# Kernel tuning notes

Hardware: AMD Instinct MI355X
Metric: run time of the kernel (lower is better)

Reference implementation:

```python
import jax, jax.numpy as jnp
import numpy as np

N = 12288      # nodes
E = 393216     # edges (avg degree 32)
D_IN = 512
D_H = 256      # interm_dim
D_Z = 64       # latent_dim


def setup_inputs() -> dict:
    key = jax.random.key(0)
    ks = jax.random.split(key, 9)
    X = jax.random.normal(ks[0], (N, D_IN), jnp.float32)
    edge_index = jax.random.randint(ks[1], (2, E), 0, N, dtype=jnp.int64)
    # GCNConv weights (glorot-ish scaling)
    W1 = jax.random.normal(ks[2], (D_IN, D_H), jnp.float32) / np.sqrt(D_IN)
    b1 = jnp.zeros((D_H,), jnp.float32)
    Wmu = jax.random.normal(ks[3], (D_H, D_Z), jnp.float32) / np.sqrt(D_H)
    bmu = jnp.zeros((D_Z,), jnp.float32)
    Wsig = jax.random.normal(ks[4], (D_H, 1), jnp.float32) / np.sqrt(D_H)
    bsig = jnp.zeros((1,), jnp.float32)
    # reparameterization noise (torch: Normal(0,1).sample(mus.size()))
    eps = jax.random.normal(ks[5], (N, D_Z), jnp.float32)
    return {"X": X, "edge_index": edge_index, "W1": W1, "b1": b1,
            "Wmu": Wmu, "bmu": bmu, "Wsig": Wsig, "bsig": bsig, "eps": eps}


def _gcn_conv(h_in, W, b, src, dst, norm):
    # GCNConv: linear transform then symmetric-normalized aggregation with self-loops
    h = h_in @ W + b                                   # [N, F_out]
    msg = h[src] * norm[src, None]                     # gather + scale
    agg = jax.ops.segment_sum(msg, dst, num_segments=N)
    # self-loop contribution: norm_i * norm_i * h_i
    return norm[:, None] * (agg + norm[:, None] * h)


def reference(X, edge_index, W1, b1, Wmu, bmu, Wsig, bsig, eps):
    src, dst = edge_index[0], edge_index[1]
    # degree of A + I (edge weight 1, plus self loop)
    deg = jax.ops.segment_sum(jnp.ones((E,), X.dtype), dst, num_segments=N) + 1.0
    norm = jax.lax.rsqrt(deg)                          # D^{-1/2}

    # encoder
    H = jax.nn.relu(_gcn_conv(X, W1, b1, src, dst, norm))   # [N, D_H]; dropout p=0.0
    mus = _gcn_conv(H, Wmu, bmu, src, dst, norm)            # [N, D_Z]
    logsigma2s = _gcn_conv(H, Wsig, bsig, src, dst, norm)   # [N, 1]

    # reparameterize
    sigmas = jnp.exp(0.5 * logsigma2s)                      # [N, 1]
    Z = mus + sigmas * eps                                  # [N, D_Z]

    # dense decoder
    ZZt = Z @ Z.T                                           # [N, N]
    return ZZt, mus, logsigma2s
```

## Files before the change

### kernel.cpp

```cpp
#include <hip/hip_runtime.h>

#define N_NODES 12288
#define N_EDGES 393216
#define DIN 512
#define DH 256
#define DZ 64

typedef __bf16 bf16x8 __attribute__((ext_vector_type(8)));
typedef float f32x4 __attribute__((ext_vector_type(4)));

static __device__ __forceinline__ unsigned short f2bf(float f) {
    unsigned int u = __float_as_uint(f);
    unsigned int r = (u + 0x7fffu + ((u >> 16) & 1u)) >> 16;
    return (unsigned short)r;
}
static __device__ __forceinline__ float bf2f(unsigned short u) {
    return __uint_as_float((unsigned int)u << 16);
}

__global__ __launch_bounds__(256) void k_prep(const float* __restrict__ X, unsigned short* __restrict__ Xb,
                                              const float* __restrict__ W1, unsigned short* __restrict__ W1T,
                                              const float* __restrict__ Wmu, unsigned short* __restrict__ WmuT,
                                              const int* __restrict__ dst, int* __restrict__ deg) {
    int b = blockIdx.x;
    if (b < 6144) {
        int i = b * 256 + threadIdx.x;
        float4 v = ((const float4*)X)[i];
        ushort4 o;
        o.x = f2bf(v.x); o.y = f2bf(v.y); o.z = f2bf(v.z); o.w = f2bf(v.w);
        ((ushort4*)Xb)[i] = o;
    } else if (b < 6656) {
        int i = (b - 6144) * 256 + threadIdx.x;
        int c = i >> 9, k = i & 511;
        W1T[i] = f2bf(W1[k * DH + c]);
    } else if (b < 6720) {
        int i = (b - 6656) * 256 + threadIdx.x;
        int c = i >> 8, k = i & 255;
        WmuT[i] = f2bf(Wmu[k * DZ + c]);
    } else {
        int e = (b - 6720) * 256 + threadIdx.x;
        atomicAdd(&deg[dst[e]], 1);
    }
}

__global__ __launch_bounds__(1024) void k_scan(const int* __restrict__ cnt, int* __restrict__ rp,
                                               float* __restrict__ norm) {
    __shared__ int sp[1024];
    int t = threadIdx.x;
    int base = t * 12;
    int loc[12];
    int s = 0;
#pragma unroll
    for (int j = 0; j < 12; ++j) {
        int c = cnt[base + j];
        norm[base + j] = rsqrtf((float)c + 1.0f);
        loc[j] = s; s += c;
    }
    sp[t] = s;
    __syncthreads();
    for (int off = 1; off < 1024; off <<= 1) {
        int v = (t >= off) ? sp[t - off] : 0;
        __syncthreads();
        sp[t] += v;
        __syncthreads();
    }
    int pre = (t == 0) ? 0 : sp[t - 1];
#pragma unroll
    for (int j = 0; j < 12; ++j) rp[base + j] = pre + loc[j];
    if (t == 1023) rp[N_NODES] = sp[1023];
}

__global__ __launch_bounds__(256) void k_scatter(const int* __restrict__ src, const int* __restrict__ dst,
                                                 const int* __restrict__ rp, int* __restrict__ cursor,
                                                 int* __restrict__ ssrc) {
    int e = blockIdx.x * 256 + threadIdx.x;
    int d = dst[e];
    int pos = atomicAdd(&cursor[d], 1);
    ssrc[rp[d] + pos] = src[e];
}

__global__ __launch_bounds__(256) void k_gemm1(const unsigned short* __restrict__ Xb,
                                               const unsigned short* __restrict__ W1T,
                                               const float* __restrict__ b1, const float* __restrict__ norm,
                                               unsigned short* __restrict__ g1) {
    int wid = threadIdx.x >> 6;
    int lane = threadIdx.x & 63;
    int ln = lane & 15, kg = lane >> 4;
    int rb = blockIdx.x * 256 + wid * 64;
    int cb = blockIdx.y * 64;
    f32x4 acc[4][4] = {};
    const unsigned short* xa = Xb + (size_t)(rb + ln) * DIN + kg * 8;
    const unsigned short* wb = W1T + (size_t)(cb + ln) * DIN + kg * 8;
    for (int ks = 0; ks < 16; ++ks) {
        int k0 = ks * 32;
        bf16x8 a[4], b[4];
#pragma unroll
        for (int m = 0; m < 4; ++m) a[m] = *(const bf16x8*)(xa + (size_t)m * 16 * DIN + k0);
#pragma unroll
        for (int n = 0; n < 4; ++n) b[n] = *(const bf16x8*)(wb + (size_t)n * 16 * DIN + k0);
#pragma unroll
        for (int m = 0; m < 4; ++m)
#pragma unroll
            for (int n = 0; n < 4; ++n)
                acc[m][n] = __builtin_amdgcn_mfma_f32_16x16x32_bf16(a[m], b[n], acc[m][n], 0, 0, 0);
    }
#pragma unroll
    for (int m = 0; m < 4; ++m)
#pragma unroll
        for (int r = 0; r < 4; ++r) {
            int row = rb + m * 16 + kg * 4 + r;
            float ni = norm[row];
#pragma unroll
            for (int n = 0; n < 4; ++n) {
                int col = cb + n * 16 + ln;
                g1[(size_t)row * DH + col] = f2bf(ni * (acc[m][n][r] + b1[col]));
            }
        }
}

__global__ __launch_bounds__(256) void k_agg1(const unsigned short* __restrict__ g1,
                                              const int* __restrict__ rp, const int* __restrict__ ssrc,
                                              const float* __restrict__ norm, const float* __restrict__ Wsig,
                                              unsigned short* __restrict__ G2, float* __restrict__ tvec,
                                              float* __restrict__ qv) {
    int w = threadIdx.x >> 6;
    int lane = threadIdx.x & 63;
    int i = blockIdx.x * 4 + w;
    int beg = rp[i], end = rp[i + 1];
    float ax = 0.f, ay = 0.f, az = 0.f, aw = 0.f;
    float ssum = 0.f;
    int co = lane << 2;
#pragma unroll 2
    for (int e = beg; e < end; ++e) {
        int s = ssrc[e];
        ushort4 v = *(const ushort4*)(g1 + ((size_t)s << 8) + co);
        ssum += norm[s];
        ax += bf2f(v.x); ay += bf2f(v.y); az += bf2f(v.z); aw += bf2f(v.w);
    }
    ushort4 sv = *(const ushort4*)(g1 + ((size_t)i << 8) + co);
    ax += bf2f(sv.x); ay += bf2f(sv.y); az += bf2f(sv.z); aw += bf2f(sv.w);
    float ni = norm[i];
    float gx = ni * fmaxf(ni * ax, 0.f);
    float gy = ni * fmaxf(ni * ay, 0.f);
    float gz = ni * fmaxf(ni * az, 0.f);
    float gw = ni * fmaxf(ni * aw, 0.f);
    ushort4 o;
    o.x = f2bf(gx); o.y = f2bf(gy); o.z = f2bf(gz); o.w = f2bf(gw);
    *(ushort4*)(G2 + ((size_t)i << 8) + co) = o;
    const float4 wsg = *(const float4*)(Wsig + co);
    float qp = gx * wsg.x + gy * wsg.y + gz * wsg.z + gw * wsg.w;
#pragma unroll
    for (int m = 32; m >= 1; m >>= 1) qp += __shfl_xor(qp, m);
#pragma unroll
    for (int m = 32; m >= 1; m >>= 1) ssum += __shfl_xor(ssum, m);
    if (lane == 0) {
        tvec[i] = ssum / 64.f + ni;
        qv[i] = qp;
    }
}

__global__ __launch_bounds__(256) void k_gemm2(const unsigned short* __restrict__ G2,
                                               const unsigned short* __restrict__ WmuT,
                                               unsigned short* __restrict__ Pb) {
    int wid = threadIdx.x >> 6;
    int lane = threadIdx.x & 63;
    int ln = lane & 15, kg = lane >> 4;
    int rb = blockIdx.x * 128 + wid * 32;
    f32x4 acc[2][4] = {};
    const unsigned short* xa = G2 + (size_t)(rb + ln) * DH + kg * 8;
    const unsigned short* wb = WmuT + (size_t)ln * DH + kg * 8;
    for (int ks = 0; ks < 8; ++ks) {
        int k0 = ks * 32;
        bf16x8 a[2], b[4];
#pragma unroll
        for (int m = 0; m < 2; ++m) a[m] = *(const bf16x8*)(xa + (size_t)m * 16 * DH + k0);
#pragma unroll
        for (int n = 0; n < 4; ++n) b[n] = *(const bf16x8*)(wb + (size_t)n * 16 * DH + k0);
#pragma unroll
        for (int m = 0; m < 2; ++m)
#pragma unroll
            for (int n = 0; n < 4; ++n)
                acc[m][n] = __builtin_amdgcn_mfma_f32_16x16x32_bf16(a[m], b[n], acc[m][n], 0, 0, 0);
    }
#pragma unroll
    for (int m = 0; m < 2; ++m)
#pragma unroll
        for (int n = 0; n < 4; ++n)
#pragma unroll
            for (int r = 0; r < 4; ++r) {
                int row = rb + m * 16 + kg * 4 + r;
                int col = n * 16 + ln;
                Pb[(size_t)row * DZ + col] = f2bf(acc[m][n][r]);
            }
}

__global__ __launch_bounds__(256) void k_agg2(const unsigned short* __restrict__ Pb,
                                              const float* __restrict__ qv,
                                              const int* __restrict__ rp, const int* __restrict__ ssrc,
                                              const float* __restrict__ norm, const float* __restrict__ tvec,
                                              const float* __restrict__ bmu, const float* __restrict__ bsig,
                                              const float* __restrict__ eps,
                                              float* __restrict__ mus_out, float* __restrict__ logs_out,
                                              unsigned short* __restrict__ Zb) {
    int w = threadIdx.x >> 6;
    int lane = threadIdx.x & 63;
    int i = blockIdx.x * 4 + w;
    int beg = rp[i], end = rp[i + 1];
    float acc = 0.f, qa = 0.f;
#pragma unroll 2
    for (int e = beg; e < end; ++e) {
        int s = ssrc[e];
        acc += bf2f(Pb[((size_t)s << 6) + lane]);
        qa += qv[s];
    }
    acc += bf2f(Pb[((size_t)i << 6) + lane]);
    qa += qv[i];
    float ni = norm[i], tv = tvec[i];
    float mu = ni * (acc + bmu[lane] * tv);
    float ls = ni * (qa + bsig[0] * tv);
    if (lane == 0) logs_out[i] = ls;
    float sig = expf(0.5f * ls);
    size_t oidx = ((size_t)i << 6) + lane;
    mus_out[oidx] = mu;
    Zb[oidx] = f2bf(mu + sig * eps[oidx]);
}

#define LPAD 260
__global__ __launch_bounds__(256) void k_zzt(const unsigned short* __restrict__ Zb, float* __restrict__ out) {
    __shared__ float lds[64 * LPAD];
    int w = threadIdx.x >> 6;
    int lane = threadIdx.x & 63;
    int ln = lane & 15, kg = lane >> 4;
    int rb = blockIdx.x * 64;
    int cb = blockIdx.y * 256 + w * 64;
    bf16x8 a[4][2], b[4][2];
#pragma unroll
    for (int m = 0; m < 4; ++m)
#pragma unroll
        for (int kc = 0; kc < 2; ++kc)
            a[m][kc] = *(const bf16x8*)(Zb + (size_t)(rb + m * 16 + ln) * DZ + kc * 32 + kg * 8);
#pragma unroll
    for (int n = 0; n < 4; ++n)
#pragma unroll
        for (int kc = 0; kc < 2; ++kc)
            b[n][kc] = *(const bf16x8*)(Zb + (size_t)(cb + n * 16 + ln) * DZ + kc * 32 + kg * 8);
    f32x4 acc[4][4] = {};
#pragma unroll
    for (int m = 0; m < 4; ++m)
#pragma unroll
        for (int n = 0; n < 4; ++n) {
            acc[m][n] = __builtin_amdgcn_mfma_f32_16x16x32_bf16(a[m][0], b[n][0], acc[m][n], 0, 0, 0);
            acc[m][n] = __builtin_amdgcn_mfma_f32_16x16x32_bf16(a[m][1], b[n][1], acc[m][n], 0, 0, 0);
        }
#pragma unroll
    for (int m = 0; m < 4; ++m)
#pragma unroll
        for (int n = 0; n < 4; ++n)
#pragma unroll
            for (int r = 0; r < 4; ++r)
                lds[(m * 16 + kg * 4 + r) * LPAD + w * 64 + n * 16 + ln] = acc[m][n][r];
    __syncthreads();
    int c4 = (threadIdx.x & 63) * 4;
    int rw = threadIdx.x >> 6;
    size_t colbase = (size_t)blockIdx.y * 256 + c4;
#pragma unroll
    for (int it = 0; it < 16; ++it) {
        int row = it * 4 + rw;
        f32x4 v = *(const f32x4*)&lds[row * LPAD + c4];
        __builtin_nontemporal_store(v, (f32x4*)(out + (size_t)(rb + row) * N_NODES + colbase));
    }
}

extern "C" void kernel_launch(void* const* d_in, const int* in_sizes, int n_in,
                              void* d_out, int out_size, void* d_ws, size_t ws_size,
                              hipStream_t stream) {
    const float* X = (const float*)d_in[0];
    const int* edge = (const int*)d_in[1];
    const float* W1 = (const float*)d_in[2];
    const float* b1 = (const float*)d_in[3];
    const float* Wmu = (const float*)d_in[4];
    const float* bmu = (const float*)d_in[5];
    const float* Wsig = (const float*)d_in[6];
    const float* bsig = (const float*)d_in[7];
    const float* eps = (const float*)d_in[8];

    const int* esrc = edge;
    const int* edst = edge + N_EDGES;

    char* w = (char*)d_ws;
    int* deg = (int*)w;            w += (size_t)N_NODES * 4;
    int* cursor = (int*)w;         w += (size_t)N_NODES * 4;
    float* norm = (float*)w;       w += (size_t)N_NODES * 4;
    float* tvec = (float*)w;       w += (size_t)N_NODES * 4;
    float* qv = (float*)w;         w += (size_t)N_NODES * 4;
    int* rowptr = (int*)w;         w += (size_t)(N_NODES + 64) * 4;
    int* ssrc = (int*)w;           w += (size_t)N_EDGES * 4;
    unsigned short* Xb = (unsigned short*)w;   w += (size_t)N_NODES * DIN * 2;
    unsigned short* W1T = (unsigned short*)w;  w += (size_t)DIN * DH * 2;
    unsigned short* WmuT = (unsigned short*)w; w += (size_t)DH * DZ * 2;
    unsigned short* g1 = (unsigned short*)w;   w += (size_t)N_NODES * DH * 2;
    unsigned short* G2 = (unsigned short*)w;   w += (size_t)N_NODES * DH * 2;
    unsigned short* Pb = (unsigned short*)w;   w += (size_t)N_NODES * DZ * 2;
    unsigned short* Zb = (unsigned short*)w;   w += (size_t)N_NODES * DZ * 2;

    float* out_zzt = (float*)d_out;
    float* out_mus = out_zzt + (size_t)N_NODES * N_NODES;
    float* out_logs = out_mus + (size_t)N_NODES * DZ;

    hipMemsetAsync(d_ws, 0, (size_t)N_NODES * 8, stream);
    k_prep<<<8256, 256, 0, stream>>>(X, Xb, W1, W1T, Wmu, WmuT, edst, deg);
    k_scan<<<1, 1024, 0, stream>>>(deg, rowptr, norm);
    k_scatter<<<N_EDGES / 256, 256, 0, stream>>>(esrc, edst, rowptr, cursor, ssrc);
    k_gemm1<<<dim3(N_NODES / 256, DH / 64), 256, 0, stream>>>(Xb, W1T, b1, norm, g1);
    k_agg1<<<N_NODES / 4, 256, 0, stream>>>(g1, rowptr, ssrc, norm, Wsig, G2, tvec, qv);
    k_gemm2<<<N_NODES / 128, 256, 0, stream>>>(G2, WmuT, Pb);
    k_agg2<<<N_NODES / 4, 256, 0, stream>>>(Pb, qv, rowptr, ssrc, norm, tvec, bmu, bsig, eps,
                                            out_mus, out_logs, Zb);
    k_zzt<<<dim3(N_NODES / 64, N_NODES / 256), 256, 0, stream>>>(Zb, out_zzt);
}
```

Before: 282.8 us.

## Split edges across wave halves in aggregations, halve ZZt LDS, widen gemm1 blocks

The aggregation kernels now process two (agg1) or four (agg2) edges at once per wave. Each lane uses a wider vector load, and partial sums are combined with cross-lane shuffles, so more gathers are in flight. The ZZt kernel stages its output through half-size LDS in two passes, which cuts shared memory per block and can allow more resident blocks, at the cost of an extra barrier. gemm1 moves to 512-thread blocks, each covering 128 columns, which changes the tiling and how many blocks are launched.

```diff
diff --git a/kernel.cpp b/kernel.cpp
--- a/kernel.cpp
+++ b/kernel.cpp
@@ -8,6 +8,7 @@
 
 typedef __bf16 bf16x8 __attribute__((ext_vector_type(8)));
 typedef float f32x4 __attribute__((ext_vector_type(4)));
+typedef unsigned short u16x8 __attribute__((ext_vector_type(8)));
 
 static __device__ __forceinline__ unsigned short f2bf(float f) {
     unsigned int u = __float_as_uint(f);
@@ -79,15 +80,15 @@
     ssrc[rp[d] + pos] = src[e];
 }
 
-__global__ __launch_bounds__(256) void k_gemm1(const unsigned short* __restrict__ Xb,
+__global__ __launch_bounds__(512) void k_gemm1(const unsigned short* __restrict__ Xb,
                                                const unsigned short* __restrict__ W1T,
                                                const float* __restrict__ b1, const float* __restrict__ norm,
                                                unsigned short* __restrict__ g1) {
     int wid = threadIdx.x >> 6;
     int lane = threadIdx.x & 63;
     int ln = lane & 15, kg = lane >> 4;
-    int rb = blockIdx.x * 256 + wid * 64;
-    int cb = blockIdx.y * 64;
+    int rb = blockIdx.x * 256 + (wid >> 1) * 64;
+    int cb = blockIdx.y * 128 + (wid & 1) * 64;
     f32x4 acc[4][4] = {};
     const unsigned short* xa = Xb + (size_t)(rb + ln) * DIN + kg * 8;
     const unsigned short* wb = W1T + (size_t)(cb + ln) * DIN + kg * 8;
@@ -125,36 +126,51 @@
                                               float* __restrict__ qv) {
     int w = threadIdx.x >> 6;
     int lane = threadIdx.x & 63;
+    int half = lane >> 5, lh = lane & 31;
     int i = blockIdx.x * 4 + w;
     int beg = rp[i], end = rp[i + 1];
-    float ax = 0.f, ay = 0.f, az = 0.f, aw = 0.f;
+    int cnt = end - beg;
+    int itn = (cnt + 1) >> 1;
+    size_t cho = (size_t)lh * 8;
+    float a8[8] = {};
     float ssum = 0.f;
-    int co = lane << 2;
 #pragma unroll 2
-    for (int e = beg; e < end; ++e) {
-        int s = ssrc[e];
-        ushort4 v = *(const ushort4*)(g1 + ((size_t)s << 8) + co);
-        ssum += norm[s];
-        ax += bf2f(v.x); ay += bf2f(v.y); az += bf2f(v.z); aw += bf2f(v.w);
-    }
-    ushort4 sv = *(const ushort4*)(g1 + ((size_t)i << 8) + co);
-    ax += bf2f(sv.x); ay += bf2f(sv.y); az += bf2f(sv.z); aw += bf2f(sv.w);
+    for (int it = 0; it < itn; ++it) {
+        int e = beg + it * 2 + half;
+        if (e < end) {
+            int s = ssrc[e];
+            u16x8 v = *(const u16x8*)(g1 + ((size_t)s << 8) + cho);
+            ssum += norm[s];
+#pragma unroll
+            for (int j = 0; j < 8; ++j) a8[j] += bf2f(v[j]);
+        }
+    }
+    if (half == 0) {
+        u16x8 v = *(const u16x8*)(g1 + ((size_t)i << 8) + cho);
+#pragma unroll
+        for (int j = 0; j < 8; ++j) a8[j] += bf2f(v[j]);
+    }
+#pragma unroll
+    for (int j = 0; j < 8; ++j) a8[j] += __shfl_xor(a8[j], 32);
+    ssum += __shfl_xor(ssum, 32);
     float ni = norm[i];
-    float gx = ni * fmaxf(ni * ax, 0.f);
-    float gy = ni * fmaxf(ni * ay, 0.f);
-    float gz = ni * fmaxf(ni * az, 0.f);
-    float gw = ni * fmaxf(ni * aw, 0.f);
-    ushort4 o;
-    o.x = f2bf(gx); o.y = f2bf(gy); o.z = f2bf(gz); o.w = f2bf(gw);
-    *(ushort4*)(G2 + ((size_t)i << 8) + co) = o;
-    const float4 wsg = *(const float4*)(Wsig + co);
-    float qp = gx * wsg.x + gy * wsg.y + gz * wsg.z + gw * wsg.w;
-#pragma unroll
-    for (int m = 32; m >= 1; m >>= 1) qp += __shfl_xor(qp, m);
-#pragma unroll
-    for (int m = 32; m >= 1; m >>= 1) ssum += __shfl_xor(ssum, m);
+    const float4 ws0 = *(const float4*)(Wsig + cho);
+    const float4 ws1 = *(const float4*)(Wsig + cho + 4);
+    float g[8];
+#pragma unroll
+    for (int j = 0; j < 8; ++j) g[j] = ni * fmaxf(ni * a8[j], 0.f);
+    float qp = g[0] * ws0.x + g[1] * ws0.y + g[2] * ws0.z + g[3] * ws0.w
+             + g[4] * ws1.x + g[5] * ws1.y + g[6] * ws1.z + g[7] * ws1.w;
+    if (half == 0) {
+        u16x8 o;
+#pragma unroll
+        for (int j = 0; j < 8; ++j) o[j] = f2bf(g[j]);
+        *(u16x8*)(G2 + ((size_t)i << 8) + cho) = o;
+    }
+#pragma unroll
+    for (int m = 16; m >= 1; m >>= 1) qp += __shfl_xor(qp, m);
     if (lane == 0) {
-        tvec[i] = ssum / 64.f + ni;
+        tvec[i] = ssum + ni;
         qv[i] = qp;
     }
 }
@@ -204,30 +220,62 @@
                                               unsigned short* __restrict__ Zb) {
     int w = threadIdx.x >> 6;
     int lane = threadIdx.x & 63;
+    int grp = lane >> 4, li = lane & 15;
     int i = blockIdx.x * 4 + w;
     int beg = rp[i], end = rp[i + 1];
-    float acc = 0.f, qa = 0.f;
+    int cnt = end - beg;
+    int itn = (cnt + 3) >> 2;
+    int co = li * 4;
+    float a4[4] = {};
+    float qa = 0.f;
 #pragma unroll 2
-    for (int e = beg; e < end; ++e) {
-        int s = ssrc[e];
-        acc += bf2f(Pb[((size_t)s << 6) + lane]);
-        qa += qv[s];
-    }
-    acc += bf2f(Pb[((size_t)i << 6) + lane]);
-    qa += qv[i];
+    for (int it = 0; it < itn; ++it) {
+        int e = beg + it * 4 + grp;
+        if (e < end) {
+            int s = ssrc[e];
+            ushort4 v = *(const ushort4*)(Pb + ((size_t)s << 6) + co);
+            qa += qv[s];
+            a4[0] += bf2f(v.x); a4[1] += bf2f(v.y); a4[2] += bf2f(v.z); a4[3] += bf2f(v.w);
+        }
+    }
+    if (grp == 0) {
+        ushort4 v = *(const ushort4*)(Pb + ((size_t)i << 6) + co);
+        qa += qv[i];
+        a4[0] += bf2f(v.x); a4[1] += bf2f(v.y); a4[2] += bf2f(v.z); a4[3] += bf2f(v.w);
+    }
+#pragma unroll
+    for (int j = 0; j < 4; ++j) {
+        a4[j] += __shfl_xor(a4[j], 16);
+        a4[j] += __shfl_xor(a4[j], 32);
+    }
+    qa += __shfl_xor(qa, 16);
+    qa += __shfl_xor(qa, 32);
     float ni = norm[i], tv = tvec[i];
-    float mu = ni * (acc + bmu[lane] * tv);
     float ls = ni * (qa + bsig[0] * tv);
+    float sig = expf(0.5f * ls);
     if (lane == 0) logs_out[i] = ls;
-    float sig = expf(0.5f * ls);
-    size_t oidx = ((size_t)i << 6) + lane;
-    mus_out[oidx] = mu;
-    Zb[oidx] = f2bf(mu + sig * eps[oidx]);
+    if (lane < 16) {
+        const float4 bm = *(const float4*)(bmu + co);
+        float4 mu;
+        mu.x = ni * (a4[0] + bm.x * tv);
+        mu.y = ni * (a4[1] + bm.y * tv);
+        mu.z = ni * (a4[2] + bm.z * tv);
+        mu.w = ni * (a4[3] + bm.w * tv);
+        size_t oidx = ((size_t)i << 6) + co;
+        *(float4*)(mus_out + oidx) = mu;
+        const float4 ep = *(const float4*)(eps + oidx);
+        ushort4 z;
+        z.x = f2bf(mu.x + sig * ep.x);
+        z.y = f2bf(mu.y + sig * ep.y);
+        z.z = f2bf(mu.z + sig * ep.z);
+        z.w = f2bf(mu.w + sig * ep.w);
+        *(ushort4*)(Zb + oidx) = z;
+    }
 }
 
 #define LPAD 260
 __global__ __launch_bounds__(256) void k_zzt(const unsigned short* __restrict__ Zb, float* __restrict__ out) {
-    __shared__ float lds[64 * LPAD];
+    __shared__ float lds[32 * LPAD];
     int w = threadIdx.x >> 6;
     int lane = threadIdx.x & 63;
     int ln = lane & 15, kg = lane >> 4;
@@ -252,22 +300,28 @@
             acc[m][n] = __builtin_amdgcn_mfma_f32_16x16x32_bf16(a[m][0], b[n][0], acc[m][n], 0, 0, 0);
             acc[m][n] = __builtin_amdgcn_mfma_f32_16x16x32_bf16(a[m][1], b[n][1], acc[m][n], 0, 0, 0);
         }
-#pragma unroll
-    for (int m = 0; m < 4; ++m)
-#pragma unroll
-        for (int n = 0; n < 4; ++n)
-#pragma unroll
-            for (int r = 0; r < 4; ++r)
-                lds[(m * 16 + kg * 4 + r) * LPAD + w * 64 + n * 16 + ln] = acc[m][n][r];
-    __syncthreads();
     int c4 = (threadIdx.x & 63) * 4;
     int rw = threadIdx.x >> 6;
     size_t colbase = (size_t)blockIdx.y * 256 + c4;
 #pragma unroll
-    for (int it = 0; it < 16; ++it) {
-        int row = it * 4 + rw;
-        f32x4 v = *(const f32x4*)&lds[row * LPAD + c4];
-        __builtin_nontemporal_store(v, (f32x4*)(out + (size_t)(rb + row) * N_NODES + colbase));
+    for (int p = 0; p < 2; ++p) {
+        if (p) __syncthreads();
+#pragma unroll
+        for (int mm = 0; mm < 2; ++mm) {
+            int m = p * 2 + mm;
+#pragma unroll
+            for (int n = 0; n < 4; ++n)
+#pragma unroll
+                for (int r = 0; r < 4; ++r)
+                    lds[(mm * 16 + kg * 4 + r) * LPAD + w * 64 + n * 16 + ln] = acc[m][n][r];
+        }
+        __syncthreads();
+#pragma unroll
+        for (int it = 0; it < 8; ++it) {
+            int rl = it * 4 + rw;
+            f32x4 v = *(const f32x4*)&lds[rl * LPAD + c4];
+            __builtin_nontemporal_store(v, (f32x4*)(out + (size_t)(rb + p * 32 + rl) * N_NODES + colbase));
+        }
     }
 }
 
@@ -311,7 +365,7 @@
     k_prep<<<8256, 256, 0, stream>>>(X, Xb, W1, W1T, Wmu, WmuT, edst, deg);
     k_scan<<<1, 1024, 0, stream>>>(deg, rowptr, norm);
     k_scatter<<<N_EDGES / 256, 256, 0, stream>>>(esrc, edst, rowptr, cursor, ssrc);
-    k_gemm1<<<dim3(N_NODES / 256, DH / 64), 256, 0, stream>>>(Xb, W1T, b1, norm, g1);
+    k_gemm1<<<dim3(N_NODES / 256, 2), 512, 0, stream>>>(Xb, W1T, b1, norm, g1);
     k_agg1<<<N_NODES / 4, 256, 0, stream>>>(g1, rowptr, ssrc, norm, Wsig, G2, tvec, qv);
     k_gemm2<<<N_NODES / 128, 256, 0, stream>>>(G2, WmuT, Pb);
     k_agg2<<<N_NODES / 4, 256, 0, stream>>>(Pb, qv, rowptr, ssrc, norm, tvec, bmu, bsig, eps,
```

New measurement: 278.4 us. Within noise of the previous version (-1.5%).
